# Performance work log

Measured on AMD Instinct MI355X. Metric: run time of the kernel, lower is better.

## Reference

```python
import jax, jax.numpy as jnp
import numpy as np

N_TOKENS = 8192
TOP_K = 2
N_EXPERTS = 8
D_MODEL = 1024
D_FF = 2048
CAPACITY = 3072  # static per-expert buffer; mean load 2048, overflow prob ~0
FP8_MAX = 448.0


def setup_inputs() -> dict:
    key = jax.random.key(0)
    ks = jax.random.split(key, 6)
    x = jax.random.normal(ks[0], (N_TOKENS, D_MODEL), dtype=jnp.float32)
    expert_indices = jax.random.randint(ks[1], (N_TOKENS, TOP_K), 0, N_EXPERTS)
    expert_weights = jax.nn.softmax(jax.random.normal(ks[2], (N_TOKENS, TOP_K)), axis=-1).astype(jnp.float32)
    # trunc_normal init, std = sqrt(1/3)/sqrt(fan_in), fan_in = w.shape[1]
    std_in = (1.0 / 3.0) ** 0.5 / D_MODEL ** 0.5
    std_ff = (1.0 / 3.0) ** 0.5 / D_FF ** 0.5
    w1 = jnp.clip(jax.random.normal(ks[3], (N_EXPERTS, D_MODEL, D_FF), jnp.float32) * std_in, -2 * std_in, 2 * std_in)
    w2 = jnp.clip(jax.random.normal(ks[4], (N_EXPERTS, D_MODEL, D_FF), jnp.float32) * std_in, -2 * std_in, 2 * std_in)
    w3 = jnp.clip(jax.random.normal(ks[5], (N_EXPERTS, D_FF, D_MODEL), jnp.float32) * std_ff, -2 * std_ff, 2 * std_ff)
    return {"x": x, "expert_indices": expert_indices, "expert_weights": expert_weights,
            "w1": w1, "w2": w2, "w3": w3}


def reference(x, expert_indices, expert_weights, w1, w2, w3):
    n_tokens, d_model = x.shape
    top_k = expert_indices.shape[1]
    n_experts = w1.shape[0]

    # input fp8 scale (buffer fill_ in torch -> no grad)
    input_scale = jax.lax.stop_gradient(FP8_MAX / (jnp.max(jnp.abs(x)) + 1e-12) * 0.9)
    # w*_scale buffers are ones at inference (recalibration happens only randomly in training)
    w_scale = jnp.float32(1.0)

    # ---- dispatch: stable sort assignments by expert, compute slot positions ----
    flat_experts = expert_indices.reshape(-1)                       # [N*K]
    flat_weights = expert_weights.reshape(-1)                       # [N*K]
    token_indices = jnp.repeat(jnp.arange(n_tokens), top_k)         # [N*K]
    order = jnp.argsort(flat_experts)                               # stable sort
    sorted_experts = flat_experts[order]
    sorted_weights = flat_weights[order]
    sorted_tokens = token_indices[order]
    counts = jnp.bincount(flat_experts, length=n_experts)           # [E]
    seg_starts = jnp.cumsum(counts) - counts                        # [E]
    positions = jnp.arange(n_tokens * top_k) - seg_starts[sorted_experts]

    # scatter tokens into padded per-expert buffers [E, CAP, d]; OOB slots dropped
    padded = jnp.zeros((n_experts, CAPACITY, d_model), x.dtype)
    padded = padded.at[sorted_experts, positions].set(x[sorted_tokens], mode='drop')

    # ---- grouped SwiGLU with fp8-style quant/dequant scaling ----
    inp_scaled = jnp.clip(padded * input_scale, -FP8_MAX, FP8_MAX)  # [E, C, d]
    w1_s = jnp.clip(w1 * w_scale, -FP8_MAX, FP8_MAX)
    w2_s = jnp.clip(w2 * w_scale, -FP8_MAX, FP8_MAX)
    w3_s = jnp.clip(w3 * w_scale, -FP8_MAX, FP8_MAX)
    gate = jnp.einsum('ecd,edf->ecf', inp_scaled, w1_s) / (input_scale * w_scale)
    gate = jax.nn.silu(gate)
    value = jnp.einsum('ecd,edf->ecf', inp_scaled, w2_s) / (input_scale * w_scale)
    hidden = gate * value                                            # [E, C, f]
    # per-expert hidden amax (padded rows are zero -> same max as valid rows)
    hidden_amax = jnp.max(jnp.abs(hidden), axis=(1, 2))              # [E]
    hidden_scale = (FP8_MAX / (hidden_amax + 1e-12) * 0.9)[:, None, None]
    hidden_scaled = jnp.clip(hidden * hidden_scale, -FP8_MAX, FP8_MAX)
    out_padded = jnp.einsum('ecf,efd->ecd', hidden_scaled, w3_s) / (hidden_scale * w_scale)

    # ---- combine: gather per-assignment outputs, weight, scatter-add per token ----
    valid = positions < CAPACITY
    gathered = out_padded[sorted_experts, jnp.minimum(positions, CAPACITY - 1)]
    gathered = gathered * jnp.where(valid, sorted_weights, 0.0)[:, None]
    output = jnp.zeros((n_tokens, d_model), x.dtype).at[sorted_tokens].add(gathered)
    return output
```

## Files before the change

### kernel.cpp

```cpp
#include <hip/hip_runtime.h>

#define N_TOK   8192
#define TOPK    2
#define N_EXP   8
#define DM      1024
#define DFF     2048
#define CAP     3072

typedef __attribute__((ext_vector_type(8))) short bf16x8;
typedef __attribute__((ext_vector_type(4))) float f32x4;

__device__ __forceinline__ unsigned short f2bf(float x) {
    union { float f; unsigned u; } un; un.f = x;
    unsigned r = un.u + 0x7fffu + ((un.u >> 16) & 1u);
    return (unsigned short)(r >> 16);
}
__device__ __forceinline__ float bf2f(unsigned short u) {
    union { unsigned u; float f; } c; c.u = ((unsigned)u) << 16; return c.f;
}

__device__ __forceinline__ void glds16(const void* g, void* l) {
    __builtin_amdgcn_global_load_lds(
        (const __attribute__((address_space(1))) unsigned int*)g,
        (__attribute__((address_space(3))) unsigned int*)l, 16, 0, 0);
}

__global__ void cvt_x_kernel(const float4* __restrict__ x, ushort4* __restrict__ xb) {
    int i = blockIdx.x * 256 + threadIdx.x;
    float4 v = x[i];
    ushort4 o;
    o.x = f2bf(v.x); o.y = f2bf(v.y); o.z = f2bf(v.z); o.w = f2bf(v.w);
    xb[i] = o;
}

__global__ void transpose_cvt64_kernel(const float* __restrict__ inA, const float* __restrict__ inB,
                                       unsigned short* __restrict__ outA, unsigned short* __restrict__ outB,
                                       int R, int C) {
    __shared__ unsigned short L[64][72];
    const int z = blockIdx.z;
    const float* in = (z & 8) ? inB : inA;
    unsigned short* out = (z & 8) ? outB : outA;
    const int e = z & 7;
    const int r0 = blockIdx.y * 64, c0 = blockIdx.x * 64;
    const int t = threadIdx.x;
    const int rr = t >> 4;
    const int cv = t & 15;
    const float4* src = (const float4*)(in + ((size_t)e * R + r0) * C + c0);
    const int c4 = C >> 2;
#pragma unroll
    for (int i = 0; i < 4; i++) {
        int r = rr + 16 * i;
        float4 v = src[(size_t)r * c4 + cv];
        L[r][cv * 4 + 0] = f2bf(v.x);
        L[r][cv * 4 + 1] = f2bf(v.y);
        L[r][cv * 4 + 2] = f2bf(v.z);
        L[r][cv * 4 + 3] = f2bf(v.w);
    }
    __syncthreads();
    unsigned short* dst = out + ((size_t)e * C + c0) * R + r0;
    const int cc = t >> 4;
    const int rv = t & 15;
#pragma unroll
    for (int i = 0; i < 4; i++) {
        int c = cc + 16 * i;
        ushort4 o;
        o.x = L[rv * 4 + 0][c];
        o.y = L[rv * 4 + 1][c];
        o.z = L[rv * 4 + 2][c];
        o.w = L[rv * 4 + 3][c];
        *(ushort4*)(dst + (size_t)c * R + rv * 4) = o;
    }
}

__global__ void dispatch_kernel(const int* __restrict__ eidx, const float* __restrict__ ewt,
                                int* __restrict__ counts, int* __restrict__ row_token,
                                float* __restrict__ row_weight, int* __restrict__ slot_of) {
    int i = blockIdx.x * 256 + threadIdx.x;
    if (i < N_TOK * TOPK) {
        int e = eidx[i];
        int pos = atomicAdd(&counts[e], 1);
        int slot = -1;
        if (pos < CAP) {
            slot = e * CAP + pos;
            row_token[slot] = i >> 1;
            row_weight[slot] = ewt[i];
        }
        slot_of[i] = slot;
    }
}


#define G1_RD_A(bc, mh) \
    _Pragma("unroll") \
    for (int _mf = 0; _mf < 4; _mf++) { \
        const char* _b = (bc) + aRow + ((mh) * 64 + _mf * 16) * 128; \
        aF[_mf][0] = *(const bf16x8*)(_b + cof0); \
        aF[_mf][1] = *(const bf16x8*)(_b + cof1); \
    }

#define G1_RD_B(bc, region, BF) \
    _Pragma("unroll") \
    for (int _ff = 0; _ff < 2; _ff++) { \
        const char* _b = (bc) + (region) + bRow + _ff * 2048; \
        BF[_ff][0] = *(const bf16x8*)(_b + cof0); \
        BF[_ff][1] = *(const bf16x8*)(_b + cof1); \
    }

#define G1_MM(ACC, mh, BF) \
    _Pragma("unroll") \
    for (int _mf = 0; _mf < 4; _mf++) \
    _Pragma("unroll") \
    for (int _ff = 0; _ff < 2; _ff++) { \
        ACC[(mh) * 4 + _mf][_ff] = __builtin_amdgcn_mfma_f32_16x16x32_bf16(aF[_mf][0], BF[_ff][0], ACC[(mh) * 4 + _mf][_ff], 0, 0, 0); \
        ACC[(mh) * 4 + _mf][_ff] = __builtin_amdgcn_mfma_f32_16x16x32_bf16(aF[_mf][1], BF[_ff][1], ACC[(mh) * 4 + _mf][_ff], 0, 0, 0); \
    }

#define G1_ST_A(bs) \
    _Pragma("unroll") \
    for (int _i = 0; _i < 4; _i++) glds16(xbc + offA[_i], (bs) + _i * 8192);

#define G1_ST_B1(bs) \
    _Pragma("unroll") \
    for (int _j = 0; _j < 2; _j++) glds16(w1c + offB[_j], (bs) + 32768 + _j * 8192);

#define G1_ST_B2(bs) \
    _Pragma("unroll") \
    for (int _j = 0; _j < 2; _j++) glds16(w2c + offB[_j], (bs) + 49152 + _j * 8192);

#define G1_BAR() do { __builtin_amdgcn_s_barrier(); asm volatile("" ::: "memory"); } while (0)

#define G1_ITER(pc, ps) do { \
    const char* bc = smem + (pc) * 65536; \
    char* bs = ldsT + (ps) * 65536; \
     \
    G1_RD_A(bc, 0); \
    G1_RD_B(bc, 32768, b1F); \
    G1_ST_A(bs); \
    asm volatile("s_waitcnt vmcnt(4)" ::: "memory"); \
    G1_BAR(); \
    __builtin_amdgcn_s_setprio(1); G1_MM(accG, 0, b1F); __builtin_amdgcn_s_setprio(0); \
    G1_BAR(); \
     \
    G1_RD_B(bc, 49152, b2F); \
    G1_ST_B1(bs); \
    G1_BAR(); \
    __builtin_amdgcn_s_setprio(1); G1_MM(accV, 0, b2F); __builtin_amdgcn_s_setprio(0); \
    G1_BAR(); \
     \
    G1_RD_A(bc, 1); \
    G1_ST_B2(bs); \
    G1_BAR(); \
    __builtin_amdgcn_s_setprio(1); G1_MM(accG, 1, b1F); __builtin_amdgcn_s_setprio(0); \
    G1_BAR(); \
     \
    asm volatile("s_waitcnt vmcnt(2)" ::: "memory"); \
    G1_BAR(); \
    __builtin_amdgcn_s_setprio(1); G1_MM(accV, 1, b2F); __builtin_amdgcn_s_setprio(0); \
    G1_BAR(); \
    _Pragma("unroll") \
    for (int _i = 0; _i < 4; _i++) offA[_i] += 128; \
    _Pragma("unroll") \
    for (int _j = 0; _j < 2; _j++) offB[_j] += 128; \
} while (0)

__global__ __launch_bounds__(512, 2)
void gemm1_kernel(const unsigned short* __restrict__ xb, const unsigned short* __restrict__ w1t,
                  const unsigned short* __restrict__ w2t, const int* __restrict__ counts,
                  const int* __restrict__ row_token, unsigned short* __restrict__ hidden) {
    const int e = blockIdx.z;
    const int r0 = blockIdx.y * 256;
    if (r0 >= counts[e]) return;
    const int f0 = blockIdx.x * 128;

    extern __shared__ char smem[];

    const int t = threadIdx.x;
    const int lane = t & 63;
    const int wave = t >> 6;
    const int wm = wave >> 2;
    const int wn = wave & 3;

    const int csrc = (((t & 7) ^ ((t >> 3) & 7)) << 4);
    const int srow = t >> 3;

    const char* xbc = (const char*)xb;
    const char* w1c = (const char*)w1t;
    const char* w2c = (const char*)w2t;
    char* ldsT = smem + t * 16;

    unsigned offA[4];
#pragma unroll
    for (int i = 0; i < 4; i++) {
        int tok = row_token[e * CAP + r0 + i * 64 + srow];
        offA[i] = (unsigned)tok * (DM * 2) + csrc;
    }
    unsigned offB[2];
#pragma unroll
    for (int j = 0; j < 2; j++)
        offB[j] = (unsigned)(e * DFF + f0 + j * 64 + srow) * (DM * 2) + csrc;

    const int l15 = lane & 15;
    const int lq = lane >> 4;
    const int swz = l15 & 7;
    const int cof0 = ((lq) ^ swz) << 4;
    const int cof1 = ((4 + lq) ^ swz) << 4;
    const int aRow = (wm * 128 + l15) * 128;
    const int bRow = (wn * 32 + l15) * 128;

    f32x4 accG[8][2], accV[8][2];
#pragma unroll
    for (int i = 0; i < 8; i++)
#pragma unroll
        for (int j = 0; j < 2; j++) {
            accG[i][j] = (f32x4){0.f, 0.f, 0.f, 0.f};
            accV[i][j] = (f32x4){0.f, 0.f, 0.f, 0.f};
        }

    bf16x8 aF[4][2], b1F[2][2], b2F[2][2];

    G1_ST_A(ldsT);
    G1_ST_B1(ldsT);
    G1_ST_B2(ldsT);
#pragma unroll
    for (int i = 0; i < 4; i++) offA[i] += 128;
#pragma unroll
    for (int j = 0; j < 2; j++) offB[j] += 128;
    asm volatile("s_waitcnt vmcnt(0)" ::: "memory");
    G1_BAR();

#pragma unroll 1
    for (int it = 0; it < 7; ++it) {
        G1_ITER(0, 1);
        G1_ITER(1, 0);
    }
    G1_ITER(0, 1);

    {
        const char* bc = smem + 65536;
        asm volatile("s_waitcnt vmcnt(0)" ::: "memory");
        G1_BAR();
        G1_RD_A(bc, 0);
        G1_RD_B(bc, 32768, b1F);
        G1_RD_B(bc, 49152, b2F);
        G1_MM(accG, 0, b1F);
        G1_MM(accV, 0, b2F);
        G1_RD_A(bc, 1);
        G1_MM(accG, 1, b1F);
        G1_MM(accV, 1, b2F);
    }

    const size_t hbase = ((size_t)e * CAP + r0) * DFF + f0;
    const int mBase = wm * 128;
    const int nBase = wn * 32;
#pragma unroll
    for (int mf = 0; mf < 8; mf++)
#pragma unroll
        for (int ff = 0; ff < 2; ff++)
#pragma unroll
            for (int r = 0; r < 4; r++) {
                int m = mBase + mf * 16 + lq * 4 + r;
                int n = nBase + ff * 16 + l15;
                float g = accG[mf][ff][r];
                float v = accV[mf][ff][r];
                float h = (g / (1.f + __expf(-g))) * v;
                hidden[hbase + (size_t)m * DFF + n] = f2bf(h);
            }
}

__global__ __launch_bounds__(256, 3)
void gemm2_kernel(const unsigned short* __restrict__ hidden, const unsigned short* __restrict__ w3t,
                  const int* __restrict__ counts, const float* __restrict__ row_weight,
                  unsigned short* __restrict__ out_rows) {
    const int e = blockIdx.z;
    const int r0 = blockIdx.y * 128;
    if (r0 >= counts[e]) return;
    const int d0 = blockIdx.x * 128;

    __shared__ unsigned short lA[128 * 32];
    __shared__ unsigned short lB[128 * 32];

    const int t = threadIdx.x;
    const int lane = t & 63;
    const int wave = t >> 6;

    const int rstage = t >> 2;
    const int cs = (t & 3) ^ ((rstage >> 1) & 3);
    const int kbyte = cs * 16;

    const char* pA0 = (const char*)(hidden + ((size_t)e * CAP + r0 + rstage) * DFF) + kbyte;
    const char* pA1 = pA0 + (size_t)64 * DFF * 2;
    const char* pB0 = (const char*)(w3t + ((size_t)e * DM + d0 + rstage) * DFF) + kbyte;
    const char* pB1 = pB0 + (size_t)64 * DFF * 2;

    char* lAp = (char*)lA + t * 16;
    char* lBp = (char*)lB + t * 16;

    const int mw = (wave & 1) * 64;
    const int nw = (wave >> 1) * 64;
    const int l15 = lane & 15;
    const int lq = lane >> 4;
    const int swz = (l15 >> 1) & 3;
    const unsigned short* aBase = lA + (mw + l15) * 32 + ((lq ^ swz) * 8);
    const unsigned short* bBase = lB + (nw + l15) * 32 + ((lq ^ swz) * 8);

    f32x4 acc[4][4];
#pragma unroll
    for (int i = 0; i < 4; i++)
#pragma unroll
        for (int j = 0; j < 4; j++) acc[i][j] = (f32x4){0.f, 0.f, 0.f, 0.f};

    for (int k0 = 0; k0 < DFF; k0 += 32) {
        glds16(pA0, lAp);  glds16(pA1, lAp + 4096);
        glds16(pB0, lBp);  glds16(pB1, lBp + 4096);
        pA0 += 64; pA1 += 64; pB0 += 64; pB1 += 64;
        __syncthreads();

        bf16x8 a[4], b[4];
#pragma unroll
        for (int i = 0; i < 4; i++) {
            a[i] = *(const bf16x8*)(aBase + i * 512);
            b[i] = *(const bf16x8*)(bBase + i * 512);
        }
#pragma unroll
        for (int i = 0; i < 4; i++)
#pragma unroll
            for (int j = 0; j < 4; j++)
                acc[i][j] = __builtin_amdgcn_mfma_f32_16x16x32_bf16(a[i], b[j], acc[i][j], 0, 0, 0);
        __syncthreads();
    }

    const float* rw = row_weight + e * CAP + r0;
#pragma unroll
    for (int i = 0; i < 4; i++)
#pragma unroll
        for (int r = 0; r < 4; r++) {
            int m = mw + i * 16 + lq * 4 + r;
            float w = rw[m];
            unsigned short* orow = out_rows + ((size_t)(e * CAP + r0 + m)) * DM + d0 + nw + l15;
#pragma unroll
            for (int j = 0; j < 4; j++)
                orow[j * 16] = f2bf(acc[i][j][r] * w);
        }
}

__global__ void combine_kernel(const int* __restrict__ slot_of,
                               const unsigned short* __restrict__ out_rows,
                               float4* __restrict__ out) {
    const int tok = blockIdx.x;
    const int t = threadIdx.x;
    const int s0 = slot_of[2 * tok];
    const int s1 = slot_of[2 * tok + 1];
    float4 acc = {0.f, 0.f, 0.f, 0.f};
    if (s0 >= 0) {
        ushort4 r = ((const ushort4*)(out_rows + (size_t)s0 * DM))[t];
        acc.x += bf2f(r.x); acc.y += bf2f(r.y); acc.z += bf2f(r.z); acc.w += bf2f(r.w);
    }
    if (s1 >= 0) {
        ushort4 r = ((const ushort4*)(out_rows + (size_t)s1 * DM))[t];
        acc.x += bf2f(r.x); acc.y += bf2f(r.y); acc.z += bf2f(r.z); acc.w += bf2f(r.w);
    }
    out[(size_t)tok * (DM / 4) + t] = acc;
}

extern "C" void kernel_launch(void* const* d_in, const int* in_sizes, int n_in,
                              void* d_out, int out_size, void* d_ws, size_t ws_size,
                              hipStream_t stream) {
    const float* x = (const float*)d_in[0];
    const int* eidx = (const int*)d_in[1];
    const float* ewt = (const float*)d_in[2];
    const float* w1 = (const float*)d_in[3];
    const float* w2 = (const float*)d_in[4];
    const float* w3 = (const float*)d_in[5];
    float* out = (float*)d_out;

    char* ws = (char*)d_ws;
    size_t off = 0;
    auto alloc = [&](size_t b) { size_t o = off; off += (b + 255) & ~(size_t)255; return o; };
    int*   counts     = (int*)(ws + alloc(N_EXP * 4));
    int*   row_token  = (int*)(ws + alloc((size_t)N_EXP * CAP * 4));
    float* row_weight = (float*)(ws + alloc((size_t)N_EXP * CAP * 4));
    size_t hdr_end = off;
    int*   slot_of    = (int*)(ws + alloc((size_t)N_TOK * TOPK * 4));
    unsigned short* xb  = (unsigned short*)(ws + alloc((size_t)N_TOK * DM * 2));
    unsigned short* w1t = (unsigned short*)(ws + alloc((size_t)N_EXP * DFF * DM * 2));
    unsigned short* w2t = (unsigned short*)(ws + alloc((size_t)N_EXP * DFF * DM * 2));
    unsigned short* w3t = (unsigned short*)(ws + alloc((size_t)N_EXP * DM * DFF * 2));
    unsigned short* hidden = (unsigned short*)(ws + alloc((size_t)N_EXP * CAP * DFF * 2));
    unsigned short* out_rows = w1t;
    (void)ws_size; (void)in_sizes; (void)n_in;

    static bool attr_done = false;
    if (!attr_done) {
        hipFuncSetAttribute((const void*)gemm1_kernel,
                            hipFuncAttributeMaxDynamicSharedMemorySize, 131072);
        attr_done = true;
    }

    hipMemsetAsync(ws, 0, hdr_end, stream);

    cvt_x_kernel<<<(N_TOK * DM / 4) / 256, 256, 0, stream>>>((const float4*)x, (ushort4*)xb);
    transpose_cvt64_kernel<<<dim3(DFF / 64, DM / 64, 16), 256, 0, stream>>>(w1, w2, w1t, w2t, DM, DFF);
    transpose_cvt64_kernel<<<dim3(DM / 64, DFF / 64, 8), 256, 0, stream>>>(w3, w3, w3t, w3t, DFF, DM);
    dispatch_kernel<<<(N_TOK * TOPK) / 256, 256, 0, stream>>>(eidx, ewt, counts, row_token, row_weight, slot_of);

    gemm1_kernel<<<dim3(DFF / 128, CAP / 256, N_EXP), 512, 131072, stream>>>(xb, w1t, w2t, counts, row_token, hidden);
    gemm2_kernel<<<dim3(DM / 128, CAP / 128, N_EXP), 256, 0, stream>>>(hidden, w3t, counts, row_weight, out_rows);
    combine_kernel<<<N_TOK, 256, 0, stream>>>(slot_of, out_rows, (float4*)out);
}
```

Measured before the change: 587.8 us.

## Repipeline gemm1 with inline-asm LDS reads and XCD-aware block mapping

Rewrites the gemm1 main loop as a software pipeline of phases. LDS fragment reads for the next MFMA group are issued with inline-asm ds_read_b128 using precomputed addresses and immediate offsets, then fenced by lgkmcnt waits and sched_barriers. Global-to-LDS stores are rebalanced across phases with finer vmcnt waits. The 3D grid becomes a 1D grid remapped so that blocks on the same XCD share an expert and f-tile, which should improve L2 reuse of weights. The risks are scheduling rigidity from the inline asm and subtle correctness in the hand-written phase ordering.

New measurement: 615.0 us. +4.6%, slower.

```diff
diff --git a/kernel.cpp b/kernel.cpp
--- a/kernel.cpp
+++ b/kernel.cpp
@@ -90,87 +90,73 @@
 }
 
 
-#define G1_RD_A(bc, mh) \
-    _Pragma("unroll") \
-    for (int _mf = 0; _mf < 4; _mf++) { \
-        const char* _b = (bc) + aRow + ((mh) * 64 + _mf * 16) * 128; \
-        aF[_mf][0] = *(const bf16x8*)(_b + cof0); \
-        aF[_mf][1] = *(const bf16x8*)(_b + cof1); \
-    }
-
-#define G1_RD_B(bc, region, BF) \
-    _Pragma("unroll") \
-    for (int _ff = 0; _ff < 2; _ff++) { \
-        const char* _b = (bc) + (region) + bRow + _ff * 2048; \
-        BF[_ff][0] = *(const bf16x8*)(_b + cof0); \
-        BF[_ff][1] = *(const bf16x8*)(_b + cof1); \
-    }
-
-#define G1_MM(ACC, mh, BF) \
-    _Pragma("unroll") \
-    for (int _mf = 0; _mf < 4; _mf++) \
-    _Pragma("unroll") \
-    for (int _ff = 0; _ff < 2; _ff++) { \
-        ACC[(mh) * 4 + _mf][_ff] = __builtin_amdgcn_mfma_f32_16x16x32_bf16(aF[_mf][0], BF[_ff][0], ACC[(mh) * 4 + _mf][_ff], 0, 0, 0); \
-        ACC[(mh) * 4 + _mf][_ff] = __builtin_amdgcn_mfma_f32_16x16x32_bf16(aF[_mf][1], BF[_ff][1], ACC[(mh) * 4 + _mf][_ff], 0, 0, 0); \
-    }
-
-#define G1_ST_A(bs) \
-    _Pragma("unroll") \
-    for (int _i = 0; _i < 4; _i++) glds16(xbc + offA[_i], (bs) + _i * 8192);
-
-#define G1_ST_B1(bs) \
-    _Pragma("unroll") \
-    for (int _j = 0; _j < 2; _j++) glds16(w1c + offB[_j], (bs) + 32768 + _j * 8192);
-
-#define G1_ST_B2(bs) \
-    _Pragma("unroll") \
-    for (int _j = 0; _j < 2; _j++) glds16(w2c + offB[_j], (bs) + 49152 + _j * 8192);
-
-#define G1_BAR() do { __builtin_amdgcn_s_barrier(); asm volatile("" ::: "memory"); } while (0)
-
-#define G1_ITER(pc, ps) do { \
-    const char* bc = smem + (pc) * 65536; \
-    char* bs = ldsT + (ps) * 65536; \
-     \
-    G1_RD_A(bc, 0); \
-    G1_RD_B(bc, 32768, b1F); \
-    G1_ST_A(bs); \
-    asm volatile("s_waitcnt vmcnt(4)" ::: "memory"); \
-    G1_BAR(); \
-    __builtin_amdgcn_s_setprio(1); G1_MM(accG, 0, b1F); __builtin_amdgcn_s_setprio(0); \
-    G1_BAR(); \
-     \
-    G1_RD_B(bc, 49152, b2F); \
-    G1_ST_B1(bs); \
-    G1_BAR(); \
-    __builtin_amdgcn_s_setprio(1); G1_MM(accV, 0, b2F); __builtin_amdgcn_s_setprio(0); \
-    G1_BAR(); \
-     \
-    G1_RD_A(bc, 1); \
-    G1_ST_B2(bs); \
-    G1_BAR(); \
-    __builtin_amdgcn_s_setprio(1); G1_MM(accG, 1, b1F); __builtin_amdgcn_s_setprio(0); \
-    G1_BAR(); \
-     \
-    asm volatile("s_waitcnt vmcnt(2)" ::: "memory"); \
-    G1_BAR(); \
-    __builtin_amdgcn_s_setprio(1); G1_MM(accV, 1, b2F); __builtin_amdgcn_s_setprio(0); \
-    G1_BAR(); \
-    _Pragma("unroll") \
-    for (int _i = 0; _i < 4; _i++) offA[_i] += 128; \
-    _Pragma("unroll") \
-    for (int _j = 0; _j < 2; _j++) offB[_j] += 128; \
+#define DSRL(dst, ar, LIT) asm volatile("ds_read_b128 %0, %1 offset:" #LIT : "=&v"(dst) : "v"(ar))
+
+#define RD_A0(B) do { \
+    DSRL(aF[0][0], adA[B][0], 0);    DSRL(aF[0][1], adA[B][1], 0); \
+    DSRL(aF[1][0], adA[B][0], 2048); DSRL(aF[1][1], adA[B][1], 2048); \
+    DSRL(aF[2][0], adA[B][0], 4096); DSRL(aF[2][1], adA[B][1], 4096); \
+    DSRL(aF[3][0], adA[B][0], 6144); DSRL(aF[3][1], adA[B][1], 6144); } while (0)
+
+#define RD_A1(B) do { \
+    DSRL(aF[0][0], adA[B][0], 8192);  DSRL(aF[0][1], adA[B][1], 8192); \
+    DSRL(aF[1][0], adA[B][0], 10240); DSRL(aF[1][1], adA[B][1], 10240); \
+    DSRL(aF[2][0], adA[B][0], 12288); DSRL(aF[2][1], adA[B][1], 12288); \
+    DSRL(aF[3][0], adA[B][0], 14336); DSRL(aF[3][1], adA[B][1], 14336); } while (0)
+
+#define RD_B1(B) do { \
+    DSRL(b1F[0][0], adB[B][0], 32768); DSRL(b1F[0][1], adB[B][1], 32768); \
+    DSRL(b1F[1][0], adB[B][0], 34816); DSRL(b1F[1][1], adB[B][1], 34816); } while (0)
+
+#define RD_B2(B) do { \
+    DSRL(b2F[0][0], adB[B][0], 49152); DSRL(b2F[0][1], adB[B][1], 49152); \
+    DSRL(b2F[1][0], adB[B][0], 51200); DSRL(b2F[1][1], adB[B][1], 51200); } while (0)
+
+#define MM(ACC, MH, BF) do { \
+    _Pragma("unroll") for (int _mf = 0; _mf < 4; _mf++) \
+    _Pragma("unroll") for (int _ff = 0; _ff < 2; _ff++) { \
+        ACC[(MH)*4+_mf][_ff] = __builtin_amdgcn_mfma_f32_16x16x32_bf16(aF[_mf][0], BF[_ff][0], ACC[(MH)*4+_mf][_ff], 0, 0, 0); \
+        ACC[(MH)*4+_mf][_ff] = __builtin_amdgcn_mfma_f32_16x16x32_bf16(aF[_mf][1], BF[_ff][1], ACC[(MH)*4+_mf][_ff], 0, 0, 0); \
+    } } while (0)
+
+#define ST_A3(bs)   do { glds16(xbc + offA[0], (bs)); glds16(xbc + offA[1], (bs) + 8192); glds16(xbc + offA[2], (bs) + 16384); } while (0)
+#define ST_A1B1(bs) do { glds16(xbc + offA[3], (bs) + 24576); glds16(w1c + offB[0], (bs) + 32768); glds16(w1c + offB[1], (bs) + 40960); } while (0)
+#define ST_B2A(bs)  do { glds16(w2c + offB[0], (bs) + 49152); glds16(w2c + offB[1], (bs) + 57344); \
+    offA[0] += 128; offA[1] += 128; offA[2] += 128; offA[3] += 128; offB[0] += 128; offB[1] += 128; } while (0)
+
+#define FENCE() asm volatile("" ::: "memory")
+#define BARX() do { FENCE(); __builtin_amdgcn_s_barrier(); FENCE(); } while (0)
+#define VMW(N) asm volatile("s_waitcnt vmcnt(" #N ")" ::: "memory")
+#define NOST ((void)0)
+#define NOWT ((void)0)
+
+#define PH(RDS, STS, MMS, WT) do { \
+    RDS; \
+    STS; \
+    BARX(); \
+    asm volatile("s_waitcnt lgkmcnt(0)" ::: "memory"); \
+    __builtin_amdgcn_sched_barrier(0); \
+    __builtin_amdgcn_s_setprio(1); \
+    MMS; \
+    __builtin_amdgcn_s_setprio(0); \
+    __builtin_amdgcn_sched_barrier(0); \
+    WT; \
+    BARX(); \
 } while (0)
 
 __global__ __launch_bounds__(512, 2)
 void gemm1_kernel(const unsigned short* __restrict__ xb, const unsigned short* __restrict__ w1t,
                   const unsigned short* __restrict__ w2t, const int* __restrict__ counts,
                   const int* __restrict__ row_token, unsigned short* __restrict__ hidden) {
-    const int e = blockIdx.z;
-    const int r0 = blockIdx.y * 256;
+    const int bid = blockIdx.x;
+    const int xcd = bid & 7;
+    const int pos = bid >> 3;
+    const int w = xcd * 192 + pos;
+    const int r0 = (w % 12) * 256;
+    const int ef = w / 12;
+    const int e = ef >> 4;
+    const int f0 = (ef & 15) * 128;
     if (r0 >= counts[e]) return;
-    const int f0 = blockIdx.x * 128;
 
     extern __shared__ char smem[];
 
@@ -186,7 +172,8 @@
     const char* xbc = (const char*)xb;
     const char* w1c = (const char*)w1t;
     const char* w2c = (const char*)w2t;
-    char* ldsT = smem + t * 16;
+    char* ldsT0 = smem + t * 16;
+    char* ldsT1 = ldsT0 + 65536;
 
     unsigned offA[4];
 #pragma unroll
@@ -204,8 +191,14 @@
     const int swz = l15 & 7;
     const int cof0 = ((lq) ^ swz) << 4;
     const int cof1 = ((4 + lq) ^ swz) << 4;
-    const int aRow = (wm * 128 + l15) * 128;
-    const int bRow = (wn * 32 + l15) * 128;
+    const unsigned ldsBase = (unsigned)(unsigned long long)smem;
+    const unsigned aRow = ldsBase + (unsigned)((wm * 128 + l15) * 128);
+    const unsigned bRow = ldsBase + (unsigned)((wn * 32 + l15) * 128);
+    unsigned adA[2][2], adB[2][2];
+    adA[0][0] = aRow + cof0;  adA[0][1] = aRow + cof1;
+    adA[1][0] = adA[0][0] + 65536;  adA[1][1] = adA[0][1] + 65536;
+    adB[0][0] = bRow + cof0;  adB[0][1] = bRow + cof1;
+    adB[1][0] = adB[0][0] + 65536;  adB[1][1] = adB[0][1] + 65536;
 
     f32x4 accG[8][2], accV[8][2];
 #pragma unroll
@@ -218,36 +211,32 @@
 
     bf16x8 aF[4][2], b1F[2][2], b2F[2][2];
 
-    G1_ST_A(ldsT);
-    G1_ST_B1(ldsT);
-    G1_ST_B2(ldsT);
-#pragma unroll
-    for (int i = 0; i < 4; i++) offA[i] += 128;
-#pragma unroll
-    for (int j = 0; j < 2; j++) offB[j] += 128;
-    asm volatile("s_waitcnt vmcnt(0)" ::: "memory");
-    G1_BAR();
+    ST_A3(ldsT0); ST_A1B1(ldsT0); ST_B2A(ldsT0);
+    VMW(2);
+    BARX();
+    RD_B1(0);
 
 #pragma unroll 1
     for (int it = 0; it < 7; ++it) {
-        G1_ITER(0, 1);
-        G1_ITER(1, 0);
-    }
-    G1_ITER(0, 1);
-
-    {
-        const char* bc = smem + 65536;
-        asm volatile("s_waitcnt vmcnt(0)" ::: "memory");
-        G1_BAR();
-        G1_RD_A(bc, 0);
-        G1_RD_B(bc, 32768, b1F);
-        G1_RD_B(bc, 49152, b2F);
-        G1_MM(accG, 0, b1F);
-        G1_MM(accV, 0, b2F);
-        G1_RD_A(bc, 1);
-        G1_MM(accG, 1, b1F);
-        G1_MM(accV, 1, b2F);
-    }
+        PH(RD_A0(0), ST_A3(ldsT1),   MM(accG, 0, b1F), VMW(3));
+        PH(RD_B2(0), ST_A1B1(ldsT1), MM(accV, 0, b2F), NOWT);
+        PH(RD_A1(0), ST_B2A(ldsT1),  MM(accG, 1, b1F), VMW(2));
+        PH(RD_B1(1), NOST,           MM(accV, 1, b2F), NOWT);
+        PH(RD_A0(1), ST_A3(ldsT0),   MM(accG, 0, b1F), VMW(3));
+        PH(RD_B2(1), ST_A1B1(ldsT0), MM(accV, 0, b2F), NOWT);
+        PH(RD_A1(1), ST_B2A(ldsT0),  MM(accG, 1, b1F), VMW(2));
+        PH(RD_B1(0), NOST,           MM(accV, 1, b2F), NOWT);
+    }
+    PH(RD_A0(0), ST_A3(ldsT1),   MM(accG, 0, b1F), VMW(3));
+    PH(RD_B2(0), ST_A1B1(ldsT1), MM(accV, 0, b2F), NOWT);
+    PH(RD_A1(0), ST_B2A(ldsT1),  MM(accG, 1, b1F), VMW(2));
+    PH(RD_B1(1), NOST,           MM(accV, 1, b2F), NOWT);
+    PH(RD_A0(1), NOST,           MM(accG, 0, b1F), VMW(0));
+    PH(RD_B2(1), NOST,           MM(accV, 0, b2F), NOWT);
+    PH(RD_A1(1), NOST,           MM(accG, 1, b1F), NOWT);
+    asm volatile("s_waitcnt lgkmcnt(0)" ::: "memory");
+    __builtin_amdgcn_sched_barrier(0);
+    MM(accV, 1, b2F);
 
     const size_t hbase = ((size_t)e * CAP + r0) * DFF + f0;
     const int mBase = wm * 128;
@@ -403,7 +392,7 @@
     transpose_cvt64_kernel<<<dim3(DM / 64, DFF / 64, 8), 256, 0, stream>>>(w3, w3, w3t, w3t, DFF, DM);
     dispatch_kernel<<<(N_TOK * TOPK) / 256, 256, 0, stream>>>(eidx, ewt, counts, row_token, row_weight, slot_of);
 
-    gemm1_kernel<<<dim3(DFF / 128, CAP / 256, N_EXP), 512, 131072, stream>>>(xb, w1t, w2t, counts, row_token, hidden);
+    gemm1_kernel<<<dim3((DFF / 128) * (CAP / 256) * N_EXP), 512, 131072, stream>>>(xb, w1t, w2t, counts, row_token, hidden);
     gemm2_kernel<<<dim3(DM / 128, CAP / 128, N_EXP), 256, 0, stream>>>(hidden, w3t, counts, row_weight, out_rows);
     combine_kernel<<<N_TOK, 256, 0, stream>>>(slot_of, out_rows, (float4*)out);
 }
```
